# Optimization experiments

Hardware: AMD Instinct MI355X
Metric: run time of the kernel (lower is better)

Reference implementation:

```python
import jax, jax.numpy as jnp
import numpy as np
from jax import lax


def loo_max(x):
    """Leave-one-out max over axis 1. x: (N, L, D) -> (N, L, D).
    Equivalent to torch's repeat + strip_main_diagonal + max(dim=2) without the
    (N, L, L, D) intermediate: for position i the LOO max is top1 unless i is
    the (unique chosen) argmax, in which case it is top2. With duplicates the
    second top-k value equals top1, so the result is still exact.
    """
    xt = jnp.swapaxes(x, 1, 2)                 # (N, D, L)
    top2, _ = lax.top_k(xt, 2)                 # (N, D, 2)
    amax = jnp.argmax(xt, axis=-1)             # (N, D)
    idx = jnp.arange(x.shape[1])[None, :, None]  # (1, L, 1)
    top1 = top2[..., 0][:, None, :]            # (N, 1, D)
    second = top2[..., 1][:, None, :]          # (N, 1, D)
    return jnp.where(idx == amax[:, None, :], second, top1)


def cross_max(y, from_length):
    """Plain max-pool over axis 1 of y, broadcast to (N, from_length, D)."""
    m = jnp.max(y, axis=1)                     # (N, D)
    return jnp.broadcast_to(m[:, None, :], (y.shape[0], from_length, y.shape[2]))


def setup_inputs() -> dict:
    key = jax.random.key(0)
    ks = jax.random.split(key, 6)
    N, L0, L1, D = 16, 2048, 1024, 128
    H = D + 2 * D  # in_dim + sum(in_dims) = 384
    scale = 1.0 / np.sqrt(H)
    return {
        "x0": jax.random.normal(ks[0], (N, L0, D), jnp.float32),
        "x1": jax.random.normal(ks[1], (N, L1, D), jnp.float32),
        "W0": jax.random.normal(ks[2], (D, H), jnp.float32) * scale,
        "b0": jax.random.normal(ks[3], (D,), jnp.float32) * scale,
        "W1": jax.random.normal(ks[4], (D, H), jnp.float32) * scale,
        "b1": jax.random.normal(ks[5], (D,), jnp.float32) * scale,
    }


def reference(x0, x1, W0, b0, W1, b1):
    L0, L1 = x0.shape[1], x1.shape[1]
    # group 0: [x0 | LOO-max(x0) | max(x1) broadcast] -> linear
    c0 = jnp.concatenate([x0, loo_max(x0), cross_max(x1, L0)], axis=-1)  # (N, L0, 384)
    y0 = jnp.einsum('nlh,oh->nlo', c0, W0) + b0                           # (N, L0, 128)
    # group 1: [x1 | max(x0) broadcast | LOO-max(x1)] -> linear
    c1 = jnp.concatenate([x1, cross_max(x0, L1), loo_max(x1)], axis=-1)  # (N, L1, 384)
    y1 = jnp.einsum('nlh,oh->nlo', c1, W1) + b1                           # (N, L1, 128)
    return (y0, y1)
```

## Files before the change

### kernel.cpp

```cpp
#include <hip/hip_runtime.h>
#include <hip/hip_bf16.h>

#define N_  16
#define L0_ 2048
#define L1_ 1024
#define D_  128
#define H_  384

#define PM1_0 0
#define PM2_0 65536
#define PAM_0 131072
#define PM1_1 196608
#define PM2_1 229376
#define PAM_1 262144
#define BASE_ 294912
#define WBF_  299008
#define HCNT_ 315392
#define HLIST_ 316160
#define XBF_  524288

typedef float  floatx4  __attribute__((ext_vector_type(4)));
typedef __bf16 bf16x8   __attribute__((ext_vector_type(8)));
typedef unsigned short ushortx8 __attribute__((ext_vector_type(8)));
typedef unsigned short ushortx4 __attribute__((ext_vector_type(4)));

__device__ __forceinline__ unsigned short f2bf(float f) {
  union { float f; unsigned int u; } v; v.f = f;
  unsigned int u = v.u;
  return (unsigned short)((u + 0x7fffu + ((u >> 16) & 1u)) >> 16);
}

__global__ __launch_bounds__(256) void stats_kernel(
    const float* __restrict__ x0, const float* __restrict__ x1,
    const float* __restrict__ W0, const float* __restrict__ W1,
    float* __restrict__ ws) {
  __shared__ float sm1[8][128], sm2[8][128];
  __shared__ int   sam[8][128];
  int bid = blockIdx.x, tid = threadIdx.x;

  if (bid >= 768) {
    int g = bid - 768;
    const float* W = g ? W1 : W0;
    unsigned short* wbf = (unsigned short*)(ws + WBF_) + g * 16384;
#pragma unroll 4
    for (int it = 0; it < 64; it++) {
      int f = tid + 256 * it;
      wbf[f] = f2bf(W[(size_t)(f >> 7) * H_ + (f & 127)]);
    }
    return;
  }

  const float* x; int n, chunk, L; float *pm1, *pm2; int* pam;
  unsigned short* xbf;
  if (bid < 512) {
    x = x0; n = bid >> 5; chunk = bid & 31; L = L0_;
    pm1 = ws + PM1_0; pm2 = ws + PM2_0; pam = (int*)ws + PAM_0;
    xbf = (unsigned short*)(ws + XBF_);
  } else {
    int b = bid - 512;
    x = x1; n = b >> 4; chunk = b & 15; L = L1_;
    pm1 = ws + PM1_1; pm2 = ws + PM2_1; pam = (int*)ws + PAM_1;
    xbf = (unsigned short*)(ws + XBF_) + (size_t)N_ * L0_ * D_;
  }
  int q = tid & 31, sub = tid >> 5;
  int lbase = chunk * 64 + sub * 8;
  const float* xp = x + (size_t)(n * L + lbase) * D_ + q * 4;
  unsigned short* xbp = xbf + (size_t)(n * L + lbase) * D_ + q * 4;

  float m1[4], m2[4]; int am[4];
#pragma unroll
  for (int j = 0; j < 4; j++) { m1[j] = -3.4e38f; m2[j] = -3.4e38f; am[j] = 0; }
#pragma unroll
  for (int r = 0; r < 8; r++) {
    float4 v = *(const float4*)(xp + (size_t)r * D_);
    float vv[4] = { v.x, v.y, v.z, v.w };
    ushortx4 bv = { f2bf(v.x), f2bf(v.y), f2bf(v.z), f2bf(v.w) };
    *(ushortx4*)(xbp + (size_t)r * D_) = bv;
    int l = lbase + r;
#pragma unroll
    for (int j = 0; j < 4; j++) {
      if (vv[j] > m1[j]) { m2[j] = m1[j]; m1[j] = vv[j]; am[j] = l; }
      else if (vv[j] > m2[j]) m2[j] = vv[j];
    }
  }
#pragma unroll
  for (int j = 0; j < 4; j++) {
    int d = q * 4 + j;
    sm1[sub][d] = m1[j]; sm2[sub][d] = m2[j]; sam[sub][d] = am[j];
  }
  __syncthreads();
  if (tid < 128) {
    int d = tid;
    float M1 = sm1[0][d], M2 = sm2[0][d]; int AM = sam[0][d];
#pragma unroll
    for (int s = 1; s < 8; s++) {
      float c1 = sm1[s][d];
      if (c1 > M1) { M2 = fmaxf(M1, sm2[s][d]); M1 = c1; AM = sam[s][d]; }
      else M2 = fmaxf(M2, c1);
    }
    int idx = (chunk * N_ + n) * D_ + d;
    pm1[idx] = M1; pm2[idx] = M2; pam[idx] = AM;
  }
}

__global__ __launch_bounds__(256) void prep_kernel(
    const float* __restrict__ W0, const float* __restrict__ b0,
    const float* __restrict__ W1, const float* __restrict__ b1,
    float* __restrict__ ws) {
  __shared__ float t1a[128], t1b[128], sdl[128], bpart[128];
  __shared__ int   sam2[128], scnt[32];
  int bid = blockIdx.x, tid = threadIdx.x;
  int g = bid >> 4, n = bid & 15;
  const float* W = g ? W1 : W0;
  const float* bias = g ? b1 : b0;

  if (tid < 32) scnt[tid] = 0;

  if (tid < 128) {
    int d = tid;
    const float* pm1 = ws + PM1_0; const float* pm2 = ws + PM2_0;
    const int* pam = (int*)ws + PAM_0;
    float M1 = pm1[n * D_ + d], M2 = pm2[n * D_ + d]; int AM = pam[n * D_ + d];
    for (int c = 1; c < 32; c++) {
      int id2 = (c * N_ + n) * D_ + d;
      float c1 = pm1[id2];
      if (c1 > M1) { M2 = fmaxf(M1, pm2[id2]); M1 = c1; AM = pam[id2]; }
      else M2 = fmaxf(M2, c1);
    }
    t1a[d] = M1;
    if (g == 0) { sdl[d] = M2 - M1; sam2[d] = AM; }
  } else {
    int d = tid - 128;
    const float* pm1 = ws + PM1_1; const float* pm2 = ws + PM2_1;
    const int* pam = (int*)ws + PAM_1;
    float M1 = pm1[n * D_ + d], M2 = pm2[n * D_ + d]; int AM = pam[n * D_ + d];
    for (int c = 1; c < 16; c++) {
      int id2 = (c * N_ + n) * D_ + d;
      float c1 = pm1[id2];
      if (c1 > M1) { M2 = fmaxf(M1, pm2[id2]); M1 = c1; AM = pam[id2]; }
      else M2 = fmaxf(M2, c1);
    }
    t1b[d] = M1;
    if (g == 1) { sdl[d] = M2 - M1; sam2[d] = AM; }
  }
  __syncthreads();

  int o = tid & 127, half = tid >> 7;
  {
    const float* wr = W + (size_t)o * H_ + 128 + half * 128;
    const float* tv = half ? t1b : t1a;
    float bsum = 0.f;
#pragma unroll 4
    for (int d = 0; d < 128; d += 4) {
      float4 wv = *(const float4*)(wr + d);
      bsum += tv[d] * wv.x + tv[d + 1] * wv.y + tv[d + 2] * wv.z + tv[d + 3] * wv.w;
    }
    if (half) { bpart[o] = bsum; }
    __syncthreads();
    if (!half) ws[BASE_ + (g * N_ + n) * D_ + o] = bias[o] + bsum + bpart[o];
  }

  if (tid < 128) {
    int d = tid; int am = sam2[d]; float dl = sdl[d];
    int t = am >> 6;
    int slot = atomicAdd(&scnt[t], 1);
    int tile = (g == 0) ? (n * 32 + t) : (512 + n * 16 + t);
    int* hl = (int*)ws + HLIST_ + tile * 256;
    hl[slot * 2]     = (am & 63) | (d << 8);
    hl[slot * 2 + 1] = __float_as_int(dl);
  }
  __syncthreads();
  int tcount = g ? 16 : 32;
  if (tid < tcount) {
    int tile = (g == 0) ? (n * 32 + tid) : (512 + n * 16 + tid);
    ((int*)ws)[HCNT_ + tile] = scnt[tid];
  }
}

__global__ __launch_bounds__(256) void gemm_kernel(
    const float* __restrict__ W0, const float* __restrict__ W1,
    float* __restrict__ out, const float* __restrict__ ws) {
  int bid = blockIdx.x, tid = threadIdx.x;
  int g, n, r0, L; const float* W; float* y; const unsigned short* xbf;
  if (bid < 512) {
    g = 0; n = bid >> 5; r0 = (bid & 31) << 6; L = L0_; W = W0; y = out;
    xbf = (const unsigned short*)(ws + XBF_);
  } else {
    int b = bid - 512; g = 1; n = b >> 4; r0 = (b & 15) << 6; L = L1_; W = W1;
    y = out + (size_t)N_ * L0_ * D_;
    xbf = (const unsigned short*)(ws + XBF_) + (size_t)N_ * L0_ * D_;
  }

  int w = tid >> 6, lane = tid & 63, lm = lane & 15, lq = lane >> 4;
  int rsub = (w & 1) << 5, cw = (w >> 1) << 6;

  int hc = ((const int*)ws)[HCNT_ + bid];
  const int* hl = (const int*)ws + HLIST_ + bid * 256;
  const float* bp = ws + BASE_ + (g * N_ + n) * D_;
  float bb[4];
#pragma unroll
  for (int j = 0; j < 4; j++) bb[j] = bp[cw + j * 16 + lm];

  const unsigned short* wbf = (const unsigned short*)(ws + WBF_) + g * 16384;
  const unsigned short* xb = xbf + (size_t)(n * L + r0 + rsub) * D_;

  floatx4 acc[2][4];
#pragma unroll
  for (int i = 0; i < 2; i++)
#pragma unroll
    for (int j = 0; j < 4; j++) acc[i][j] = (floatx4){0.f, 0.f, 0.f, 0.f};

#pragma unroll 2
  for (int kk = 0; kk < 4; kk++) {
    int ko = kk * 32 + lq * 8;
    bf16x8 af[2];
#pragma unroll
    for (int i = 0; i < 2; i++)
      af[i] = __builtin_bit_cast(bf16x8,
          *(const ushortx8*)(xb + (size_t)(i * 16 + lm) * D_ + ko));
    bf16x8 bfr[4];
#pragma unroll
    for (int j = 0; j < 4; j++)
      bfr[j] = __builtin_bit_cast(bf16x8,
          *(const ushortx8*)&wbf[(cw + j * 16 + lm) * 128 + ko]);
#pragma unroll
    for (int i = 0; i < 2; i++)
#pragma unroll
      for (int j = 0; j < 4; j++)
        acc[i][j] = __builtin_amdgcn_mfma_f32_16x16x32_bf16(af[i], bfr[j], acc[i][j], 0, 0, 0);
  }

  int off = 128 + (g << 7);
  for (int k = 0; k < hc; k++) {
    int e = hl[2 * k]; float dl = __int_as_float(hl[2 * k + 1]);
    int row = e & 63, d = e >> 8;
    int rl = row - rsub;
    if (rl >= 0 && rl < 32 && ((rl >> 2) & 3) == lq) {
      int i = rl >> 4, rr = rl & 3;
#pragma unroll
      for (int j = 0; j < 4; j++)
        acc[i][j][rr] += dl * W[(size_t)(cw + j * 16 + lm) * H_ + off + d];
    }
  }

  float* yb = y + (size_t)(n * L + r0 + rsub) * D_;
#pragma unroll
  for (int i = 0; i < 2; i++)
#pragma unroll
    for (int j = 0; j < 4; j++)
#pragma unroll
      for (int r = 0; r < 4; r++)
        yb[(size_t)(i * 16 + lq * 4 + r) * D_ + cw + j * 16 + lm] = acc[i][j][r] + bb[j];
}

extern "C" void kernel_launch(void* const* d_in, const int* in_sizes, int n_in,
                              void* d_out, int out_size, void* d_ws, size_t ws_size,
                              hipStream_t stream) {
  const float* x0 = (const float*)d_in[0];
  const float* x1 = (const float*)d_in[1];
  const float* W0 = (const float*)d_in[2];
  const float* b0 = (const float*)d_in[3];
  const float* W1 = (const float*)d_in[4];
  const float* b1 = (const float*)d_in[5];
  float* out = (float*)d_out;
  float* ws  = (float*)d_ws;

  hipLaunchKernelGGL(stats_kernel, dim3(770), dim3(256), 0, stream, x0, x1, W0, W1, ws);
  hipLaunchKernelGGL(prep_kernel,  dim3(32),  dim3(256), 0, stream, W0, b0, W1, b1, ws);
  hipLaunchKernelGGL(gemm_kernel,  dim3(768), dim3(256), 0, stream, W0, W1, out, ws);
}
```

Measured before the change: 140.4 us.

## Fuse prep stage into GEMM kernel, recomputing per-block stats in shared memory

Removes the separate 32-block prep kernel. Each of the 768 GEMM blocks now reduces the per-chunk max/second-max/argmax partials itself, computes the broadcast bias row, and builds its own LOO correction list in shared memory. This drops a kernel launch and a serialization point along with the workspace round-trip for the base and hit lists. In exchange, every block repeats the reduction and the 128x256 bias dot product, which adds redundant global reads and compute in front of the MFMA loop.

```diff
diff --git a/kernel.cpp b/kernel.cpp
--- a/kernel.cpp
+++ b/kernel.cpp
@@ -13,10 +13,7 @@
 #define PM1_1 196608
 #define PM2_1 229376
 #define PAM_1 262144
-#define BASE_ 294912
 #define WBF_  299008
-#define HCNT_ 315392
-#define HLIST_ 316160
 #define XBF_  524288
 
 typedef float  floatx4  __attribute__((ext_vector_type(4)));
@@ -103,45 +100,55 @@
   }
 }
 
-__global__ __launch_bounds__(256) void prep_kernel(
+__global__ __launch_bounds__(256) void gemm_kernel(
     const float* __restrict__ W0, const float* __restrict__ b0,
     const float* __restrict__ W1, const float* __restrict__ b1,
-    float* __restrict__ ws) {
-  __shared__ float t1a[128], t1b[128], sdl[128], bpart[128];
-  __shared__ int   sam2[128], scnt[32];
+    float* __restrict__ out, const float* __restrict__ ws) {
+  __shared__ float t1a[128], t1b[128], sdl[128], bpart[128], sbase[128], slda[128];
+  __shared__ int   sam2[128], slist[128], scnt;
   int bid = blockIdx.x, tid = threadIdx.x;
-  int g = bid >> 4, n = bid & 15;
-  const float* W = g ? W1 : W0;
-  const float* bias = g ? b1 : b0;
-
-  if (tid < 32) scnt[tid] = 0;
-
-  if (tid < 128) {
-    int d = tid;
-    const float* pm1 = ws + PM1_0; const float* pm2 = ws + PM2_0;
-    const int* pam = (int*)ws + PAM_0;
-    float M1 = pm1[n * D_ + d], M2 = pm2[n * D_ + d]; int AM = pam[n * D_ + d];
-    for (int c = 1; c < 32; c++) {
-      int id2 = (c * N_ + n) * D_ + d;
-      float c1 = pm1[id2];
-      if (c1 > M1) { M2 = fmaxf(M1, pm2[id2]); M1 = c1; AM = pam[id2]; }
-      else M2 = fmaxf(M2, c1);
-    }
-    t1a[d] = M1;
-    if (g == 0) { sdl[d] = M2 - M1; sam2[d] = AM; }
+  int g, n, t, L; const float *W, *bias; float* y; const unsigned short* xbf;
+  if (bid < 512) {
+    g = 0; n = bid >> 5; t = bid & 31; L = L0_; W = W0; bias = b0; y = out;
+    xbf = (const unsigned short*)(ws + XBF_);
   } else {
-    int d = tid - 128;
-    const float* pm1 = ws + PM1_1; const float* pm2 = ws + PM2_1;
-    const int* pam = (int*)ws + PAM_1;
-    float M1 = pm1[n * D_ + d], M2 = pm2[n * D_ + d]; int AM = pam[n * D_ + d];
-    for (int c = 1; c < 16; c++) {
-      int id2 = (c * N_ + n) * D_ + d;
-      float c1 = pm1[id2];
-      if (c1 > M1) { M2 = fmaxf(M1, pm2[id2]); M1 = c1; AM = pam[id2]; }
-      else M2 = fmaxf(M2, c1);
-    }
-    t1b[d] = M1;
-    if (g == 1) { sdl[d] = M2 - M1; sam2[d] = AM; }
+    int b = bid - 512; g = 1; n = b >> 4; t = b & 15; L = L1_; W = W1; bias = b1;
+    y = out + (size_t)N_ * L0_ * D_;
+    xbf = (const unsigned short*)(ws + XBF_) + (size_t)N_ * L0_ * D_;
+  }
+  int r0 = t << 6;
+
+  if (tid == 0) scnt = 0;
+
+  {
+    int d = tid & 127;
+    if (tid < 128) {
+      const float* pm1 = ws + PM1_0; const float* pm2 = ws + PM2_0;
+      const int* pam = (const int*)ws + PAM_0;
+      float M1 = pm1[n * D_ + d], M2 = pm2[n * D_ + d]; int AM = pam[n * D_ + d];
+#pragma unroll 8
+      for (int c = 1; c < 32; c++) {
+        int id2 = (c * N_ + n) * D_ + d;
+        float c1 = pm1[id2];
+        if (c1 > M1) { M2 = fmaxf(M1, pm2[id2]); M1 = c1; AM = pam[id2]; }
+        else M2 = fmaxf(M2, c1);
+      }
+      t1a[d] = M1;
+      if (g == 0) { sdl[d] = M2 - M1; sam2[d] = AM; }
+    } else {
+      const float* pm1 = ws + PM1_1; const float* pm2 = ws + PM2_1;
+      const int* pam = (const int*)ws + PAM_1;
+      float M1 = pm1[n * D_ + d], M2 = pm2[n * D_ + d]; int AM = pam[n * D_ + d];
+#pragma unroll 8
+      for (int c = 1; c < 16; c++) {
+        int id2 = (c * N_ + n) * D_ + d;
+        float c1 = pm1[id2];
+        if (c1 > M1) { M2 = fmaxf(M1, pm2[id2]); M1 = c1; AM = pam[id2]; }
+        else M2 = fmaxf(M2, c1);
+      }
+      t1b[d] = M1;
+      if (g == 1) { sdl[d] = M2 - M1; sam2[d] = AM; }
+    }
   }
   __syncthreads();
 
@@ -151,55 +158,31 @@
     const float* tv = half ? t1b : t1a;
     float bsum = 0.f;
 #pragma unroll 4
-    for (int d = 0; d < 128; d += 4) {
-      float4 wv = *(const float4*)(wr + d);
-      bsum += tv[d] * wv.x + tv[d + 1] * wv.y + tv[d + 2] * wv.z + tv[d + 3] * wv.w;
-    }
-    if (half) { bpart[o] = bsum; }
+    for (int d2 = 0; d2 < 128; d2 += 4) {
+      float4 wv = *(const float4*)(wr + d2);
+      bsum += tv[d2] * wv.x + tv[d2 + 1] * wv.y + tv[d2 + 2] * wv.z + tv[d2 + 3] * wv.w;
+    }
+    if (half) bpart[o] = bsum;
+    if (tid < 128) {
+      int am = sam2[tid];
+      if ((am >> 6) == t) {
+        int slot = atomicAdd(&scnt, 1);
+        slist[slot] = (am & 63) | (tid << 8);
+        slda[slot] = sdl[tid];
+      }
+    }
     __syncthreads();
-    if (!half) ws[BASE_ + (g * N_ + n) * D_ + o] = bias[o] + bsum + bpart[o];
-  }
-
-  if (tid < 128) {
-    int d = tid; int am = sam2[d]; float dl = sdl[d];
-    int t = am >> 6;
-    int slot = atomicAdd(&scnt[t], 1);
-    int tile = (g == 0) ? (n * 32 + t) : (512 + n * 16 + t);
-    int* hl = (int*)ws + HLIST_ + tile * 256;
-    hl[slot * 2]     = (am & 63) | (d << 8);
-    hl[slot * 2 + 1] = __float_as_int(dl);
+    if (!half) sbase[o] = bias[o] + bsum + bpart[o];
   }
   __syncthreads();
-  int tcount = g ? 16 : 32;
-  if (tid < tcount) {
-    int tile = (g == 0) ? (n * 32 + tid) : (512 + n * 16 + tid);
-    ((int*)ws)[HCNT_ + tile] = scnt[tid];
-  }
-}
-
-__global__ __launch_bounds__(256) void gemm_kernel(
-    const float* __restrict__ W0, const float* __restrict__ W1,
-    float* __restrict__ out, const float* __restrict__ ws) {
-  int bid = blockIdx.x, tid = threadIdx.x;
-  int g, n, r0, L; const float* W; float* y; const unsigned short* xbf;
-  if (bid < 512) {
-    g = 0; n = bid >> 5; r0 = (bid & 31) << 6; L = L0_; W = W0; y = out;
-    xbf = (const unsigned short*)(ws + XBF_);
-  } else {
-    int b = bid - 512; g = 1; n = b >> 4; r0 = (b & 15) << 6; L = L1_; W = W1;
-    y = out + (size_t)N_ * L0_ * D_;
-    xbf = (const unsigned short*)(ws + XBF_) + (size_t)N_ * L0_ * D_;
-  }
 
   int w = tid >> 6, lane = tid & 63, lm = lane & 15, lq = lane >> 4;
   int rsub = (w & 1) << 5, cw = (w >> 1) << 6;
 
-  int hc = ((const int*)ws)[HCNT_ + bid];
-  const int* hl = (const int*)ws + HLIST_ + bid * 256;
-  const float* bp = ws + BASE_ + (g * N_ + n) * D_;
+  int hc = scnt;
   float bb[4];
 #pragma unroll
-  for (int j = 0; j < 4; j++) bb[j] = bp[cw + j * 16 + lm];
+  for (int j = 0; j < 4; j++) bb[j] = sbase[cw + j * 16 + lm];
 
   const unsigned short* wbf = (const unsigned short*)(ws + WBF_) + g * 16384;
   const unsigned short* xb = xbf + (size_t)(n * L + r0 + rsub) * D_;
@@ -232,7 +215,7 @@
 
   int off = 128 + (g << 7);
   for (int k = 0; k < hc; k++) {
-    int e = hl[2 * k]; float dl = __int_as_float(hl[2 * k + 1]);
+    int e = slist[k]; float dl = slda[k];
     int row = e & 63, d = e >> 8;
     int rl = row - rsub;
     if (rl >= 0 && rl < 32 && ((rl >> 2) & 3) == lq) {
@@ -266,6 +249,6 @@
   float* ws  = (float*)d_ws;
 
   hipLaunchKernelGGL(stats_kernel, dim3(770), dim3(256), 0, stream, x0, x1, W0, W1, ws);
-  hipLaunchKernelGGL(prep_kernel,  dim3(32),  dim3(256), 0, stream, W0, b0, W1, b1, ws);
-  hipLaunchKernelGGL(gemm_kernel,  dim3(768), dim3(256), 0, stream, W0, W1, out, ws);
-}
+  hipLaunchKernelGGL(gemm_kernel,  dim3(768), dim3(256), 0, stream,
+                     W0, b0, W1, b1, out, ws);
+}
```

Result: slower. 148.4 us (+5.7%).

## Swap MFMA operands for vectorized output stores and pack partial stats

Applied to the files above, without the earlier changes.

The GEMM swaps its MFMA A/B operands so each lane holds four consecutive output columns. The epilogue can then write floatx4 nontemporal stores instead of scalar strided stores, and the bias and hit-correction indexing are adjusted to match the transposed fragment layout. Partial max/second-max/argmax are packed into one 16-byte record so the reduction does single vector loads, and x reads use nontemporal loads. The cost is a larger workspace and a per-hit correction loop that now reads four W rows per lane instead of one.

```diff
diff --git a/kernel.cpp b/kernel.cpp
--- a/kernel.cpp
+++ b/kernel.cpp
@@ -7,17 +7,13 @@
 #define D_  128
 #define H_  384
 
-#define PM1_0 0
-#define PM2_0 65536
-#define PAM_0 131072
-#define PM1_1 196608
-#define PM2_1 229376
-#define PAM_1 262144
-#define BASE_ 294912
-#define WBF_  299008
-#define HCNT_ 315392
-#define HLIST_ 316160
-#define XBF_  524288
+#define PMQ_0 0
+#define PMQ_1 262144
+#define BASE_ 393216
+#define WBF_  397312
+#define HCNT_ 413696
+#define HLIST_ 414464
+#define XBF_  655360
 
 typedef float  floatx4  __attribute__((ext_vector_type(4)));
 typedef __bf16 bf16x8   __attribute__((ext_vector_type(8)));
@@ -50,16 +46,16 @@
     return;
   }
 
-  const float* x; int n, chunk, L; float *pm1, *pm2; int* pam;
+  const float* x; int n, chunk, L; floatx4* pmq;
   unsigned short* xbf;
   if (bid < 512) {
     x = x0; n = bid >> 5; chunk = bid & 31; L = L0_;
-    pm1 = ws + PM1_0; pm2 = ws + PM2_0; pam = (int*)ws + PAM_0;
+    pmq = (floatx4*)(ws + PMQ_0);
     xbf = (unsigned short*)(ws + XBF_);
   } else {
     int b = bid - 512;
     x = x1; n = b >> 4; chunk = b & 15; L = L1_;
-    pm1 = ws + PM1_1; pm2 = ws + PM2_1; pam = (int*)ws + PAM_1;
+    pmq = (floatx4*)(ws + PMQ_1);
     xbf = (unsigned short*)(ws + XBF_) + (size_t)N_ * L0_ * D_;
   }
   int q = tid & 31, sub = tid >> 5;
@@ -72,15 +68,15 @@
   for (int j = 0; j < 4; j++) { m1[j] = -3.4e38f; m2[j] = -3.4e38f; am[j] = 0; }
 #pragma unroll
   for (int r = 0; r < 8; r++) {
-    float4 v = *(const float4*)(xp + (size_t)r * D_);
-    float vv[4] = { v.x, v.y, v.z, v.w };
-    ushortx4 bv = { f2bf(v.x), f2bf(v.y), f2bf(v.z), f2bf(v.w) };
+    floatx4 v = __builtin_nontemporal_load((const floatx4*)(xp + (size_t)r * D_));
+    ushortx4 bv = { f2bf(v[0]), f2bf(v[1]), f2bf(v[2]), f2bf(v[3]) };
     *(ushortx4*)(xbp + (size_t)r * D_) = bv;
     int l = lbase + r;
 #pragma unroll
     for (int j = 0; j < 4; j++) {
-      if (vv[j] > m1[j]) { m2[j] = m1[j]; m1[j] = vv[j]; am[j] = l; }
-      else if (vv[j] > m2[j]) m2[j] = vv[j];
+      float vj = v[j];
+      if (vj > m1[j]) { m2[j] = m1[j]; m1[j] = vj; am[j] = l; }
+      else if (vj > m2[j]) m2[j] = vj;
     }
   }
 #pragma unroll
@@ -98,8 +94,8 @@
       if (c1 > M1) { M2 = fmaxf(M1, sm2[s][d]); M1 = c1; AM = sam[s][d]; }
       else M2 = fmaxf(M2, c1);
     }
-    int idx = (chunk * N_ + n) * D_ + d;
-    pm1[idx] = M1; pm2[idx] = M2; pam[idx] = AM;
+    floatx4 outv = { M1, M2, __int_as_float(AM), 0.f };
+    pmq[(chunk * N_ + n) * D_ + d] = outv;
   }
 }
 
@@ -118,26 +114,28 @@
 
   if (tid < 128) {
     int d = tid;
-    const float* pm1 = ws + PM1_0; const float* pm2 = ws + PM2_0;
-    const int* pam = (int*)ws + PAM_0;
-    float M1 = pm1[n * D_ + d], M2 = pm2[n * D_ + d]; int AM = pam[n * D_ + d];
+    const floatx4* pmq = (const floatx4*)(ws + PMQ_0);
+    floatx4 v = pmq[n * D_ + d];
+    float M1 = v[0], M2 = v[1]; int AM = __float_as_int(v[2]);
+#pragma unroll 8
     for (int c = 1; c < 32; c++) {
-      int id2 = (c * N_ + n) * D_ + d;
-      float c1 = pm1[id2];
-      if (c1 > M1) { M2 = fmaxf(M1, pm2[id2]); M1 = c1; AM = pam[id2]; }
+      floatx4 u = pmq[(c * N_ + n) * D_ + d];
+      float c1 = u[0];
+      if (c1 > M1) { M2 = fmaxf(M1, u[1]); M1 = c1; AM = __float_as_int(u[2]); }
       else M2 = fmaxf(M2, c1);
     }
     t1a[d] = M1;
     if (g == 0) { sdl[d] = M2 - M1; sam2[d] = AM; }
   } else {
     int d = tid - 128;
-    const float* pm1 = ws + PM1_1; const float* pm2 = ws + PM2_1;
-    const int* pam = (int*)ws + PAM_1;
-    float M1 = pm1[n * D_ + d], M2 = pm2[n * D_ + d]; int AM = pam[n * D_ + d];
+    const floatx4* pmq = (const floatx4*)(ws + PMQ_1);
+    floatx4 v = pmq[n * D_ + d];
+    float M1 = v[0], M2 = v[1]; int AM = __float_as_int(v[2]);
+#pragma unroll 8
     for (int c = 1; c < 16; c++) {
-      int id2 = (c * N_ + n) * D_ + d;
-      float c1 = pm1[id2];
-      if (c1 > M1) { M2 = fmaxf(M1, pm2[id2]); M1 = c1; AM = pam[id2]; }
+      floatx4 u = pmq[(c * N_ + n) * D_ + d];
+      float c1 = u[0];
+      if (c1 > M1) { M2 = fmaxf(M1, u[1]); M1 = c1; AM = __float_as_int(u[2]); }
       else M2 = fmaxf(M2, c1);
     }
     t1b[d] = M1;
@@ -197,9 +195,10 @@
   int hc = ((const int*)ws)[HCNT_ + bid];
   const int* hl = (const int*)ws + HLIST_ + bid * 256;
   const float* bp = ws + BASE_ + (g * N_ + n) * D_;
-  float bb[4];
-#pragma unroll
-  for (int j = 0; j < 4; j++) bb[j] = bp[cw + j * 16 + lm];
+  floatx4 bb[4];
+#pragma unroll
+  for (int j = 0; j < 4; j++)
+    bb[j] = *(const floatx4*)&bp[cw + j * 16 + lq * 4];
 
   const unsigned short* wbf = (const unsigned short*)(ws + WBF_) + g * 16384;
   const unsigned short* xb = xbf + (size_t)(n * L + r0 + rsub) * D_;
@@ -227,7 +226,7 @@
     for (int i = 0; i < 2; i++)
 #pragma unroll
       for (int j = 0; j < 4; j++)
-        acc[i][j] = __builtin_amdgcn_mfma_f32_16x16x32_bf16(af[i], bfr[j], acc[i][j], 0, 0, 0);
+        acc[i][j] = __builtin_amdgcn_mfma_f32_16x16x32_bf16(bfr[j], af[i], acc[i][j], 0, 0, 0);
   }
 
   int off = 128 + (g << 7);
@@ -235,11 +234,13 @@
     int e = hl[2 * k]; float dl = __int_as_float(hl[2 * k + 1]);
     int row = e & 63, d = e >> 8;
     int rl = row - rsub;
-    if (rl >= 0 && rl < 32 && ((rl >> 2) & 3) == lq) {
-      int i = rl >> 4, rr = rl & 3;
+    if (rl >= 0 && rl < 32 && lm == (rl & 15)) {
+      int i = rl >> 4;
 #pragma unroll
       for (int j = 0; j < 4; j++)
-        acc[i][j][rr] += dl * W[(size_t)(cw + j * 16 + lm) * H_ + off + d];
+#pragma unroll
+        for (int r = 0; r < 4; r++)
+          acc[i][j][r] += dl * W[(size_t)(cw + j * 16 + lq * 4 + r) * H_ + off + d];
     }
   }
 
@@ -247,10 +248,11 @@
 #pragma unroll
   for (int i = 0; i < 2; i++)
 #pragma unroll
-    for (int j = 0; j < 4; j++)
-#pragma unroll
-      for (int r = 0; r < 4; r++)
-        yb[(size_t)(i * 16 + lq * 4 + r) * D_ + cw + j * 16 + lm] = acc[i][j][r] + bb[j];
+    for (int j = 0; j < 4; j++) {
+      floatx4 v = acc[i][j] + bb[j];
+      __builtin_nontemporal_store(v,
+          (floatx4*)&yb[(size_t)(i * 16 + lm) * D_ + cw + j * 16 + lq * 4]);
+    }
 }
 
 extern "C" void kernel_launch(void* const* d_in, const int* in_sizes, int n_in,
```

After: 217.9 us. +55.2%, slower.
